# Performance work log

Measured on AMD Instinct MI355X. Metric: run time of the kernel, lower is better.

## Reference

```python
import jax, jax.numpy as jnp
import numpy as np

DIM = 1024
NUM_HEADS = 16
HEAD_DIM = DIM // NUM_HEADS
SCALE = HEAD_DIM ** -0.5


def setup_inputs() -> dict:
    key = jax.random.key(0)
    k_x, k_qw, k_qb, k_pw, k_pb = jax.random.split(key, 5)
    B, N = 4, 4096
    x = jax.random.normal(k_x, (B, N, DIM), dtype=jnp.float32)
    # nn.Linear(dim, 3*dim): weight (out, in), bias (out,)
    s = DIM ** -0.5
    qkv_w = jax.random.uniform(k_qw, (3 * DIM, DIM), jnp.float32, -s, s)
    qkv_b = jax.random.uniform(k_qb, (3 * DIM,), jnp.float32, -s, s)
    proj_w = jax.random.uniform(k_pw, (DIM, DIM), jnp.float32, -s, s)
    proj_b = jax.random.uniform(k_pb, (DIM,), jnp.float32, -s, s)
    return {"x": x, "qkv_w": qkv_w, "qkv_b": qkv_b,
            "proj_w": proj_w, "proj_b": proj_b}


def reference(x, qkv_w, qkv_b, proj_w, proj_b):
    B, N, C = x.shape
    H, D = NUM_HEADS, HEAD_DIM
    # qkv projection: (B,N,3C) -> (B,N,3,H,D)
    qkv = (jnp.einsum('bnc,oc->bno', x, qkv_w) + qkv_b).reshape(B, N, 3, H, D)
    q, k, v = qkv[:, :, 0], qkv[:, :, 1], qkv[:, :, 2]  # each (B,N,H,D)
    # Faithful to source: matmul over the last two dims of (B,N,H,D),
    # i.e. attention scores over the HEAD axis per token -> (B,N,H,H).
    attn = jnp.einsum('bnhd,bngd->bnhg', q, k) * SCALE
    attn = jax.nn.softmax(attn, axis=-1)
    out = jnp.einsum('bnhg,bngd->bnhd', attn, v)      # (B,N,H,D)
    # torch: .transpose(1,2).reshape(B,N,C) -> (B,H,N,D) reshaped to (B,N,C)
    out = out.transpose(0, 2, 1, 3).reshape(B, N, C)
    return jnp.einsum('bnc,oc->bno', out, proj_w) + proj_b
```

## Files before the change

kernel.cpp:

```cpp
#include <hip/hip_runtime.h>
#include <hip/hip_bf16.h>

#define TOK   16384
#define KD    1024
#define NQKV  3072
#define SEQL  4096
#define ATT_SCALE 0.125f

typedef __attribute__((ext_vector_type(4))) float f32x4;
typedef __attribute__((ext_vector_type(8))) short bf16x8;

__device__ __forceinline__ unsigned short f2b(float f){
    union { float f; unsigned u; } x; x.f = f;
    return (unsigned short)((x.u + 0x7FFFu + ((x.u >> 16) & 1u)) >> 16);
}
__device__ __forceinline__ float b2f(unsigned short s){
    union { unsigned u; float f; } x; x.u = ((unsigned)s) << 16;
    return x.f;
}
__device__ __forceinline__ bf16x8 lds8(const unsigned short* p){
    union { uint4 u; bf16x8 v; } t; t.u = *(const uint4*)p; return t.v;
}
__device__ __forceinline__ void glds16(const void* g, void* l){
    __builtin_amdgcn_global_load_lds((const __attribute__((address_space(1))) unsigned*)g,
                                     (__attribute__((address_space(3))) unsigned*)l, 16, 0, 0);
}

__global__ __launch_bounds__(256) void cvt_kernel(const float* __restrict__ in,
                                                  unsigned short* __restrict__ out, int n)
{
    int i = (blockIdx.x * 256 + threadIdx.x) * 8;
    if (i >= n) return;
    float4 a = *(const float4*)(in + i);
    float4 b = *(const float4*)(in + i + 4);
    union { unsigned short u[8]; uint4 v; } t;
    t.u[0]=f2b(a.x); t.u[1]=f2b(a.y); t.u[2]=f2b(a.z); t.u[3]=f2b(a.w);
    t.u[4]=f2b(b.x); t.u[5]=f2b(b.y); t.u[6]=f2b(b.z); t.u[7]=f2b(b.w);
    *(uint4*)(out + i) = t.v;
}

template<bool OUT_BF16>
__global__ __launch_bounds__(512, 2) void gemm256(const unsigned short* __restrict__ A,
        const unsigned short* __restrict__ Bw, const float* __restrict__ bias,
        void* __restrict__ Cp, int Nn)
{
    extern __shared__ unsigned short smem[];
    unsigned short* As = smem;
    unsigned short* Bs = smem + 32768;

    const int tid = threadIdx.x, lane = tid & 63;
    const int w = tid >> 6, wm = w >> 2, wn = w & 3;
    const int rl = lane & 15, kslot = lane >> 4;

    const int gx = gridDim.x;
    const int nwg = gx * gridDim.y;
    int id = blockIdx.y * gx + blockIdx.x;
    id = (id & 7) * (nwg >> 3) + (id >> 3);
    const int cBase = (id % gx) * 256;
    const int mBase = (id / gx) * 256;

    const int u = tid >> 3;
    const int seg8 = ((tid & 7) ^ (u & 7)) * 8;
    const unsigned short* Ag = A  + (size_t)(mBase + u) * KD + seg8;
    const unsigned short* Bg = Bw + (size_t)(cBase + (u >> 4) * 64 + (u & 15)) * KD + seg8;

    const int arow = (wm * 16 + rl) * 64;
    const int brow = (wn * 16 + rl) * 64;
    const int psg0 = (kslot ^ (rl & 7)) * 8;
    const int psg1 = ((kslot + 4) ^ (rl & 7)) * 8;

    f32x4 acc[8][4];
    #pragma unroll
    for (int m = 0; m < 8; m++)
        #pragma unroll
        for (int n = 0; n < 4; n++) acc[m][n] = (f32x4)0.f;

#define STAGE_AH0(bb, kk) { glds16(Ag + (kk),            As + (bb)*16384 + tid*8); \
                            glds16(Ag + 64*KD + (kk),    As + (bb)*16384 + 4096  + tid*8); }
#define STAGE_AH1(bb, kk) { glds16(Ag + 128*KD + (kk),   As + (bb)*16384 + 8192  + tid*8); \
                            glds16(Ag + 192*KD + (kk),   As + (bb)*16384 + 12288 + tid*8); }
#define STAGE_BH0(bb, kk) { glds16(Bg + (kk),            Bs + (bb)*16384 + tid*8); \
                            glds16(Bg + 16*KD + (kk),    Bs + (bb)*16384 + 4096  + tid*8); }
#define STAGE_BH1(bb, kk) { glds16(Bg + 32*KD + (kk),    Bs + (bb)*16384 + 8192  + tid*8); \
                            glds16(Bg + 48*KD + (kk),    Bs + (bb)*16384 + 12288 + tid*8); }

#define RDA(a_, half) { _Pragma("unroll") \
    for (int m = 0; m < 4; m++) { \
        af[m][0] = lds8((a_) + (half)*8192 + arow + m*2048 + psg0); \
        af[m][1] = lds8((a_) + (half)*8192 + arow + m*2048 + psg1); } }
#define RDB(b_, nlo) { _Pragma("unroll") \
    for (int n = 0; n < 2; n++) { \
        bf[(nlo)+n][0] = lds8((b_) + brow + ((nlo)+n)*4096 + psg0); \
        bf[(nlo)+n][1] = lds8((b_) + brow + ((nlo)+n)*4096 + psg1); } }

#define MM16(mb, nb) { \
    __builtin_amdgcn_s_setprio(1); \
    _Pragma("unroll") \
    for (int m = 0; m < 4; m++) \
        _Pragma("unroll") \
        for (int n = 0; n < 2; n++) { \
            acc[(mb)+m][(nb)+n] = __builtin_amdgcn_mfma_f32_16x16x32_bf16(af[m][0], bf[(nb)+n][0], acc[(mb)+m][(nb)+n], 0, 0, 0); \
            acc[(mb)+m][(nb)+n] = __builtin_amdgcn_mfma_f32_16x16x32_bf16(af[m][1], bf[(nb)+n][1], acc[(mb)+m][(nb)+n], 0, 0, 0); } \
    __builtin_amdgcn_s_setprio(0); }

#define WAITLGKM { asm volatile("s_waitcnt lgkmcnt(0)" ::: "memory"); __builtin_amdgcn_sched_barrier(0); }

    bf16x8 af[4][2], bf[4][2];

    STAGE_AH0(0, 0)
    STAGE_BH0(0, 0)
    STAGE_BH1(0, 0)
    STAGE_AH1(0, 0)

    int buf = 0;
    for (int t = 0; t < 15; ++t) {
        const unsigned short* a = As + buf * 16384;
        const unsigned short* b = Bs + buf * 16384;
        const int nk = (t + 1) * 64;
        STAGE_AH0(buf ^ 1, nk)
        asm volatile("s_waitcnt vmcnt(6)" ::: "memory");
        __builtin_amdgcn_s_barrier();
        RDA(a, 0) RDB(b, 0)
        WAITLGKM
        MM16(0, 0)
        STAGE_BH0(buf ^ 1, nk)
        asm volatile("s_waitcnt vmcnt(6)" ::: "memory");
        __builtin_amdgcn_s_barrier();
        RDB(b, 2)
        WAITLGKM
        MM16(0, 2)
        STAGE_BH1(buf ^ 1, nk)
        asm volatile("s_waitcnt vmcnt(6)" ::: "memory");
        __builtin_amdgcn_s_barrier();
        RDA(a, 1)
        WAITLGKM
        MM16(4, 0)
        STAGE_AH1(buf ^ 1, nk)
        MM16(4, 2)
        buf ^= 1;
    }
    {
        const unsigned short* a = As + buf * 16384;
        const unsigned short* b = Bs + buf * 16384;
        asm volatile("s_waitcnt vmcnt(4)" ::: "memory");
        __builtin_amdgcn_s_barrier();
        RDA(a, 0) RDB(b, 0)
        WAITLGKM
        MM16(0, 0)
        asm volatile("s_waitcnt vmcnt(2)" ::: "memory");
        __builtin_amdgcn_s_barrier();
        RDB(b, 2)
        WAITLGKM
        MM16(0, 2)
        asm volatile("s_waitcnt vmcnt(0)" ::: "memory");
        __builtin_amdgcn_s_barrier();
        RDA(a, 1)
        WAITLGKM
        MM16(4, 0)
        MM16(4, 2)
    }
#undef STAGE_AH0
#undef STAGE_AH1
#undef STAGE_BH0
#undef STAGE_BH1
#undef RDA
#undef RDB
#undef MM16
#undef WAITLGKM

    float bv[4];
    #pragma unroll
    for (int n = 0; n < 4; n++) bv[n] = bias[cBase + wn * 64 + n * 16 + rl];
    #pragma unroll
    for (int m = 0; m < 8; m++) {
        #pragma unroll
        for (int i = 0; i < 4; i++) {
            const size_t row = mBase + (m >> 2) * 128 + (m & 3) * 32 + wm * 16 + kslot * 4 + i;
            #pragma unroll
            for (int n = 0; n < 4; n++) {
                const int col = cBase + wn * 64 + n * 16 + rl;
                const float val = acc[m][n][i] + bv[n];
                if (OUT_BF16) ((unsigned short*)Cp)[row * Nn + col] = f2b(val);
                else          ((float*)Cp)[row * Nn + col] = val;
            }
        }
    }
}

__global__ __launch_bounds__(256) void attn_kernel(const unsigned short* __restrict__ qkv,
                                                   unsigned short* __restrict__ outp)
{
    __shared__ __align__(16) unsigned short qs[4][48 * 72];
    __shared__ float ps[4][16 * 17];
    const int tid = threadIdx.x, w = tid >> 6, lane = tid & 63;
    const int t = blockIdx.x * 4 + w;

    const unsigned short* src = qkv + (size_t)t * NQKV;
    #pragma unroll
    for (int i = 0; i < 6; i++) {
        const int e = i * 512 + lane * 8;
        uint4 v = *(const uint4*)(src + e);
        *(uint4*)&qs[w][(e >> 6) * 72 + (e & 63)] = v;
    }
    __syncthreads();

    const int h = lane & 15, g0 = lane >> 4;
    uint4 qv[8];
    #pragma unroll
    for (int i = 0; i < 8; i++) qv[i] = *(const uint4*)&qs[w][h * 72 + i * 8];
    float s[4];
    #pragma unroll
    for (int i = 0; i < 4; i++) {
        const int g = g0 * 4 + i;
        float a = 0.f;
        #pragma unroll
        for (int c = 0; c < 8; c++) {
            uint4 kv = *(const uint4*)&qs[w][(16 + g) * 72 + c * 8];
            uint qa[4] = {qv[c].x, qv[c].y, qv[c].z, qv[c].w};
            uint ka[4] = {kv.x, kv.y, kv.z, kv.w};
            #pragma unroll
            for (int uu = 0; uu < 4; uu++) {
                a += b2f((unsigned short)qa[uu]) * b2f((unsigned short)ka[uu]);
                a += b2f((unsigned short)(qa[uu] >> 16)) * b2f((unsigned short)(ka[uu] >> 16));
            }
        }
        s[i] = a * ATT_SCALE;
    }
    float mx = fmaxf(fmaxf(s[0], s[1]), fmaxf(s[2], s[3]));
    mx = fmaxf(mx, __shfl_xor(mx, 16, 64));
    mx = fmaxf(mx, __shfl_xor(mx, 32, 64));
    float p[4], smv = 0.f;
    #pragma unroll
    for (int i = 0; i < 4; i++) { p[i] = __expf(s[i] - mx); smv += p[i]; }
    smv += __shfl_xor(smv, 16, 64);
    smv += __shfl_xor(smv, 32, 64);
    const float inv = 1.f / smv;
    #pragma unroll
    for (int i = 0; i < 4; i++) ps[w][h * 17 + g0 * 4 + i] = p[i] * inv;
    __syncthreads();

    const int h2 = lane >> 2, db = (lane & 3) * 16;
    float pr[16];
    #pragma unroll
    for (int g = 0; g < 16; g++) pr[g] = ps[w][h2 * 17 + g];
    float acc[16];
    #pragma unroll
    for (int j = 0; j < 16; j++) acc[j] = 0.f;
    #pragma unroll
    for (int g = 0; g < 16; g++) {
        const unsigned short* vp = &qs[w][(32 + g) * 72 + db];
        uint4 v0 = *(const uint4*)vp;
        uint4 v1 = *(const uint4*)(vp + 8);
        const float pg = pr[g];
        uint va[8] = {v0.x, v0.y, v0.z, v0.w, v1.x, v1.y, v1.z, v1.w};
        #pragma unroll
        for (int uu = 0; uu < 8; uu++) {
            acc[2*uu]   += pg * b2f((unsigned short)va[uu]);
            acc[2*uu+1] += pg * b2f((unsigned short)(va[uu] >> 16));
        }
    }
    const int b = t >> 12, n = t & 4095;
    const int n1 = h2 * 256 + (n >> 4);
    const int c0 = (n & 15) * 64 + db;
    union { unsigned short u[16]; uint4 v[2]; } st;
    #pragma unroll
    for (int j = 0; j < 16; j++) st.u[j] = f2b(acc[j]);
    unsigned short* dst = outp + ((size_t)(b * SEQL + n1)) * 1024 + c0;
    *(uint4*)dst       = st.v[0];
    *(uint4*)(dst + 8) = st.v[1];
}

extern "C" void kernel_launch(void* const* d_in, const int* in_sizes, int n_in,
                              void* d_out, int out_size, void* d_ws, size_t ws_size,
                              hipStream_t stream)
{
    const float* x      = (const float*)d_in[0];
    const float* qkv_w  = (const float*)d_in[1];
    const float* qkv_b  = (const float*)d_in[2];
    const float* proj_w = (const float*)d_in[3];
    const float* proj_b = (const float*)d_in[4];

    unsigned short* xb  = (unsigned short*)d_ws;
    unsigned short* qkv = xb + (size_t)TOK * KD;
    unsigned short* qwb = qkv + (size_t)TOK * NQKV;
    unsigned short* pwb = qwb + (size_t)NQKV * KD;
    unsigned short* att = xb;

    hipFuncSetAttribute(reinterpret_cast<const void*>(&gemm256<true>),
                        hipFuncAttributeMaxDynamicSharedMemorySize, 131072);
    hipFuncSetAttribute(reinterpret_cast<const void*>(&gemm256<false>),
                        hipFuncAttributeMaxDynamicSharedMemorySize, 131072);

    cvt_kernel<<<dim3(TOK * KD / 2048), dim3(256), 0, stream>>>(x, xb, TOK * KD);
    cvt_kernel<<<dim3(NQKV * KD / 2048), dim3(256), 0, stream>>>(qkv_w, qwb, NQKV * KD);
    cvt_kernel<<<dim3(KD * KD / 2048), dim3(256), 0, stream>>>(proj_w, pwb, KD * KD);

    gemm256<true><<<dim3(NQKV / 256, TOK / 256), dim3(512), 131072, stream>>>(
        xb, qwb, qkv_b, qkv, NQKV);
    attn_kernel<<<dim3(TOK / 4), dim3(256), 0, stream>>>(qkv, att);
    gemm256<false><<<dim3(KD / 256, TOK / 256), dim3(512), 131072, stream>>>(
        att, pwb, proj_b, (float*)d_out, KD);
}
```

Measured before the change: 201.1 us.

## Merge conversion launches and double-buffer B fragments to drop explicit LDS waits

The three fp32-to-bf16 conversion launches become one kernel that selects its source and destination by block index, removing two launch gaps. In the GEMM main loop, the B fragments are split into two separate register sets and the explicit lgkmcnt(0) waits with scheduling barriers are removed. This lets the compiler overlap LDS reads with MFMA issue and reuse the first B half for the second A half. The cost is more live registers under the 512x2 launch bounds, and the scheduling now depends on the compiler inserting the correct waits.

```diff
diff --git a/kernel.cpp b/kernel.cpp
--- a/kernel.cpp
+++ b/kernel.cpp
@@ -26,17 +26,23 @@
                                      (__attribute__((address_space(3))) unsigned*)l, 16, 0, 0);
 }
 
-__global__ __launch_bounds__(256) void cvt_kernel(const float* __restrict__ in,
-                                                  unsigned short* __restrict__ out, int n)
+__global__ __launch_bounds__(256) void cvt3_kernel(const float* __restrict__ x,
+        const float* __restrict__ qw, const float* __restrict__ pw,
+        unsigned short* __restrict__ xb, unsigned short* __restrict__ qwb,
+        unsigned short* __restrict__ pwb)
 {
-    int i = (blockIdx.x * 256 + threadIdx.x) * 8;
-    if (i >= n) return;
-    float4 a = *(const float4*)(in + i);
-    float4 b = *(const float4*)(in + i + 4);
+    const int b = blockIdx.x;
+    const float* src; unsigned short* dst; int off;
+    if (b < 8192)       { src = x;  dst = xb;  off = b; }
+    else if (b < 9728)  { src = qw; dst = qwb; off = b - 8192; }
+    else                { src = pw; dst = pwb; off = b - 9728; }
+    const int i = (off * 256 + threadIdx.x) * 8;
+    float4 a = *(const float4*)(src + i);
+    float4 c = *(const float4*)(src + i + 4);
     union { unsigned short u[8]; uint4 v; } t;
     t.u[0]=f2b(a.x); t.u[1]=f2b(a.y); t.u[2]=f2b(a.z); t.u[3]=f2b(a.w);
-    t.u[4]=f2b(b.x); t.u[5]=f2b(b.y); t.u[6]=f2b(b.z); t.u[7]=f2b(b.w);
-    *(uint4*)(out + i) = t.v;
+    t.u[4]=f2b(c.x); t.u[5]=f2b(c.y); t.u[6]=f2b(c.z); t.u[7]=f2b(c.w);
+    *(uint4*)(dst + i) = t.v;
 }
 
 template<bool OUT_BF16>
@@ -88,24 +94,25 @@
     for (int m = 0; m < 4; m++) { \
         af[m][0] = lds8((a_) + (half)*8192 + arow + m*2048 + psg0); \
         af[m][1] = lds8((a_) + (half)*8192 + arow + m*2048 + psg1); } }
-#define RDB(b_, nlo) { _Pragma("unroll") \
+#define RDB(b_, nlo, BF) { _Pragma("unroll") \
     for (int n = 0; n < 2; n++) { \
-        bf[(nlo)+n][0] = lds8((b_) + brow + ((nlo)+n)*4096 + psg0); \
-        bf[(nlo)+n][1] = lds8((b_) + brow + ((nlo)+n)*4096 + psg1); } }
-
-#define MM16(mb, nb) { \
+        BF[n][0] = lds8((b_) + brow + ((nlo)+n)*4096 + psg0); \
+        BF[n][1] = lds8((b_) + brow + ((nlo)+n)*4096 + psg1); } }
+
+#define MM16(mb, nb, BF) { \
     __builtin_amdgcn_s_setprio(1); \
     _Pragma("unroll") \
     for (int m = 0; m < 4; m++) \
         _Pragma("unroll") \
         for (int n = 0; n < 2; n++) { \
-            acc[(mb)+m][(nb)+n] = __builtin_amdgcn_mfma_f32_16x16x32_bf16(af[m][0], bf[(nb)+n][0], acc[(mb)+m][(nb)+n], 0, 0, 0); \
-            acc[(mb)+m][(nb)+n] = __builtin_amdgcn_mfma_f32_16x16x32_bf16(af[m][1], bf[(nb)+n][1], acc[(mb)+m][(nb)+n], 0, 0, 0); } \
+            acc[(mb)+m][(nb)+n] = __builtin_amdgcn_mfma_f32_16x16x32_bf16(af[m][0], BF[n][0], acc[(mb)+m][(nb)+n], 0, 0, 0); \
+            acc[(mb)+m][(nb)+n] = __builtin_amdgcn_mfma_f32_16x16x32_bf16(af[m][1], BF[n][1], acc[(mb)+m][(nb)+n], 0, 0, 0); } \
     __builtin_amdgcn_s_setprio(0); }
 
-#define WAITLGKM { asm volatile("s_waitcnt lgkmcnt(0)" ::: "memory"); __builtin_amdgcn_sched_barrier(0); }
-
-    bf16x8 af[4][2], bf[4][2];
+#define VMC(N)  asm volatile("s_waitcnt vmcnt(" #N ")" ::: "memory");
+#define BARR    __builtin_amdgcn_s_barrier();
+
+    bf16x8 af[4][2], bfP[2][2], bfQ[2][2];
 
     STAGE_AH0(0, 0)
     STAGE_BH0(0, 0)
@@ -118,46 +125,40 @@
         const unsigned short* b = Bs + buf * 16384;
         const int nk = (t + 1) * 64;
         STAGE_AH0(buf ^ 1, nk)
-        asm volatile("s_waitcnt vmcnt(6)" ::: "memory");
-        __builtin_amdgcn_s_barrier();
-        RDA(a, 0) RDB(b, 0)
-        WAITLGKM
-        MM16(0, 0)
+        VMC(6)
+        BARR
+        RDA(a, 0) RDB(b, 0, bfP)
+        MM16(0, 0, bfP)
         STAGE_BH0(buf ^ 1, nk)
-        asm volatile("s_waitcnt vmcnt(6)" ::: "memory");
-        __builtin_amdgcn_s_barrier();
-        RDB(b, 2)
-        WAITLGKM
-        MM16(0, 2)
+        VMC(6)
+        BARR
+        RDB(b, 2, bfQ)
+        MM16(0, 2, bfQ)
         STAGE_BH1(buf ^ 1, nk)
-        asm volatile("s_waitcnt vmcnt(6)" ::: "memory");
-        __builtin_amdgcn_s_barrier();
+        VMC(6)
+        BARR
         RDA(a, 1)
-        WAITLGKM
-        MM16(4, 0)
+        MM16(4, 0, bfP)
         STAGE_AH1(buf ^ 1, nk)
-        MM16(4, 2)
+        MM16(4, 2, bfQ)
         buf ^= 1;
     }
     {
         const unsigned short* a = As + buf * 16384;
         const unsigned short* b = Bs + buf * 16384;
-        asm volatile("s_waitcnt vmcnt(4)" ::: "memory");
-        __builtin_amdgcn_s_barrier();
-        RDA(a, 0) RDB(b, 0)
-        WAITLGKM
-        MM16(0, 0)
-        asm volatile("s_waitcnt vmcnt(2)" ::: "memory");
-        __builtin_amdgcn_s_barrier();
-        RDB(b, 2)
-        WAITLGKM
-        MM16(0, 2)
-        asm volatile("s_waitcnt vmcnt(0)" ::: "memory");
-        __builtin_amdgcn_s_barrier();
+        VMC(4)
+        BARR
+        RDA(a, 0) RDB(b, 0, bfP)
+        MM16(0, 0, bfP)
+        VMC(2)
+        BARR
+        RDB(b, 2, bfQ)
+        MM16(0, 2, bfQ)
+        VMC(0)
+        BARR
         RDA(a, 1)
-        WAITLGKM
-        MM16(4, 0)
-        MM16(4, 2)
+        MM16(4, 0, bfP)
+        MM16(4, 2, bfQ)
     }
 #undef STAGE_AH0
 #undef STAGE_AH1
@@ -166,7 +167,8 @@
 #undef RDA
 #undef RDB
 #undef MM16
-#undef WAITLGKM
+#undef VMC
+#undef BARR
 
     float bv[4];
     #pragma unroll
@@ -291,9 +293,7 @@
     hipFuncSetAttribute(reinterpret_cast<const void*>(&gemm256<false>),
                         hipFuncAttributeMaxDynamicSharedMemorySize, 131072);
 
-    cvt_kernel<<<dim3(TOK * KD / 2048), dim3(256), 0, stream>>>(x, xb, TOK * KD);
-    cvt_kernel<<<dim3(NQKV * KD / 2048), dim3(256), 0, stream>>>(qkv_w, qwb, NQKV * KD);
-    cvt_kernel<<<dim3(KD * KD / 2048), dim3(256), 0, stream>>>(proj_w, pwb, KD * KD);
+    cvt3_kernel<<<dim3(10240), dim3(256), 0, stream>>>(x, qkv_w, proj_w, xb, qwb, pwb);
 
     gemm256<true><<<dim3(NQKV / 256, TOK / 256), dim3(512), 131072, stream>>>(
         xb, qwb, qkv_b, qkv, NQKV);
```

Result: faster. 196.7 us (-2.2%).
